# Performance work log

Measured on AMD Instinct MI355X. Metric: run time of the kernel, lower is better.

## Reference

```python
import jax, jax.numpy as jnp
import numpy as np

K = 3  # adaptive kernel size
M = 4  # channel reduction


def setup_inputs() -> dict:
    key = jax.random.key(0)
    ks = jax.random.split(key, 10)
    N, C, H, W = 32, 512, 48, 48
    Cm = C // M            # 128
    P = 512                # planes
    sc = 0.05
    x   = jax.random.normal(ks[0], (N, C, H, W), jnp.float32)
    Wc  = jax.random.normal(ks[1], (Cm, C), jnp.float32) * sc   # conv 1x1 (C->Cm)
    bc  = jax.random.normal(ks[2], (Cm,), jnp.float32) * sc
    Wkk = jax.random.normal(ks[3], (K * K,), jnp.float32) * sc  # conv_kernel (1->k*k, 1x1)
    bkk = jax.random.normal(ks[4], (K * K,), jnp.float32) * sc
    Wck = jax.random.normal(ks[5], (Cm, 2), jnp.float32) * sc   # conv_k (2->Cm, 1x1)
    bck = jax.random.normal(ks[6], (Cm,), jnp.float32) * sc
    b_ad = jax.random.normal(ks[7], (Cm,), jnp.float32) * sc    # conv_adap_kernel bias (learned)
    Wf  = jax.random.normal(ks[8], (P, Cm), jnp.float32) * sc   # fuse 1x1 (Cm->planes)
    bf  = jax.random.normal(ks[9], (P,), jnp.float32) * sc
    return {"x": x, "Wc": Wc, "bc": bc, "Wkk": Wkk, "bkk": bkk,
            "Wck": Wck, "bck": bck, "b_ad": b_ad, "Wf": Wf, "bf": bf}


def reference(x, Wc, bc, Wkk, bkk, Wck, bck, b_ad, Wf, bf):
    N, C, H, W = x.shape
    Cm = Wc.shape[0]
    k = K
    pad = (k - 1) // 2

    # f = relu(conv1x1(x)) -> [N, Cm, H, W]
    f = jax.nn.relu(jnp.einsum('oc,nchw->nohw', Wc, x) + bc[None, :, None, None])

    # global branch: adaptive avg pool to 1 -> shared conv1x1 -> relu -> [N, Cm]
    gk1 = jax.nn.relu(jnp.mean(x, axis=(2, 3)) @ Wc.T + bc)
    # conv_kernel (1->k*k 1x1 over permuted layout): per-channel affine into k*k values
    g_kern = (gk1[:, :, None] * Wkk[None, None, :] + bkk[None, None, :]).reshape(N, Cm, k, k)

    # spatial branch: adaptive max pool to k x k (H,W divisible by k) -> shared conv1x1 -> relu
    xm = x.reshape(N, C, k, H // k, k, W // k).max(axis=(3, 5))  # [N, C, k, k]
    sk = jax.nn.relu(jnp.einsum('oc,nckl->nokl', Wc, xm) + bc[None, :, None, None])

    # kernel generation: conv_k (2->Cm 1x1) over [g_kern, sk], then the permute makes
    # weight[o, c, :, :] = relu(sum_j Wck[o, j] * gs[c, j, :, :] + bck[o])
    gs = jnp.stack([g_kern, sk], axis=2)  # [N, Cm, 2, k, k]
    dynW = jax.nn.relu(jnp.einsum('oj,ncjkl->nockl', Wck, gs)
                       + bck[None, :, None, None, None])  # [N, Cm_out, Cm_in, k, k]

    # per-sample dynamic conv2d, vectorized over batch
    def conv_one(fn, wn):
        return jax.lax.conv_general_dilated(
            fn[None], wn, window_strides=(1, 1),
            padding=[(pad, pad), (pad, pad)])[0]

    y = jax.vmap(conv_one)(f, dynW) + b_ad[None, :, None, None]  # [N, Cm, H, W]

    # fuse 1x1 -> planes
    out = jnp.einsum('oc,nchw->nohw', Wf, y) + bf[None, :, None, None]
    return out
```

## Files before the change

### kernel.cpp

```cpp
#include <hip/hip_runtime.h>

#define N_   32
#define C_   512
#define CM_  128
#define H_   48
#define W_   48
#define HW_  (H_*W_)
#define P_   512

typedef unsigned short ushort_t;
typedef short s8v  __attribute__((ext_vector_type(8)));
typedef float f4v  __attribute__((ext_vector_type(4)));

__device__ __forceinline__ ushort_t f2bf(float x) {
    unsigned int u = __float_as_uint(x);
    u += 0x7fffu + ((u >> 16) & 1u);
    return (ushort_t)(u >> 16);
}

__global__ __launch_bounds__(256) void pool_kernel(const float* __restrict__ x,
                                                   float* __restrict__ meanx,
                                                   float* __restrict__ xm,
                                                   const float* __restrict__ Wc,
                                                   const float* __restrict__ Wf,
                                                   ushort_t* __restrict__ Wc_bf,
                                                   ushort_t* __restrict__ Wf_bf) {
    if (blockIdx.x >= N_ * C_) {
        int idx = (blockIdx.x - N_ * C_) * 256 + threadIdx.x;
        float4 v;
        ushort_t* dst;
        if (idx < 16384) {
            v = ((const float4*)Wc)[idx];
            dst = Wc_bf + (size_t)idx * 4;
        } else {
            int k = idx - 16384;
            v = ((const float4*)Wf)[k];
            dst = Wf_bf + (size_t)k * 4;
        }
        uint2 pk;
        pk.x = (unsigned)f2bf(v.x) | ((unsigned)f2bf(v.y) << 16);
        pk.y = (unsigned)f2bf(v.z) | ((unsigned)f2bf(v.w) << 16);
        *(uint2*)dst = pk;
        return;
    }
    int plane = blockIdx.x;
    const float* base = x + (size_t)plane * HW_;
    int t = threadIdx.x;
    int r = t >> 4, cc = t & 15;
    float sum = 0.f;
    float mx[9];
#pragma unroll
    for (int b = 0; b < 9; ++b) {
        int h = (b / 3) * 16 + r;
        int w = (b % 3) * 16 + cc;
        float v = base[h * W_ + w];
        mx[b] = v;
        sum += v;
    }
#pragma unroll
    for (int off = 32; off > 0; off >>= 1) {
        sum += __shfl_down(sum, off);
#pragma unroll
        for (int b = 0; b < 9; ++b) mx[b] = fmaxf(mx[b], __shfl_down(mx[b], off));
    }
    __shared__ float s[4][10];
    int wave = t >> 6, lane = t & 63;
    if (lane == 0) {
#pragma unroll
        for (int b = 0; b < 9; ++b) s[wave][b] = mx[b];
        s[wave][9] = sum;
    }
    __syncthreads();
    if (t < 9) {
        float v = fmaxf(fmaxf(s[0][t], s[1][t]), fmaxf(s[2][t], s[3][t]));
        xm[(size_t)plane * 9 + t] = v;
    } else if (t == 9) {
        float v = s[0][9] + s[1][9] + s[2][9] + s[3][9];
        meanx[plane] = v * (1.0f / (float)HW_);
    }
}

__global__ __launch_bounds__(512) void branch_kernel(const float* __restrict__ meanx,
                                                     const float* __restrict__ xm,
                                                     const float* __restrict__ Wc,
                                                     const float* __restrict__ bc,
                                                     const float* __restrict__ Wkk,
                                                     const float* __restrict__ bkk,
                                                     float* __restrict__ gs) {
    int n = blockIdx.x;
    __shared__ float sin_[C_ * 10];
    __shared__ float Ws[4][128][17];
    int t = threadIdx.x;
    for (int i = t; i < C_ * 10; i += 512) {
        int c = i / 10, j = i % 10;
        sin_[i] = (j < 9) ? xm[((size_t)n * C_ + c) * 9 + j] : meanx[n * C_ + c];
    }
    int o = t & 127, p = t >> 7;
    float acc[10];
#pragma unroll
    for (int j = 0; j < 10; ++j) acc[j] = 0.f;

    for (int s = 0; s < 8; ++s) {
        __syncthreads();
#pragma unroll
        for (int k = 0; k < 4; ++k) {
            int f = t + k * 512;
            int chunk = f >> 9, oo = (f >> 2) & 127, col4 = f & 3;
            float4 v = *(const float4*)(Wc + (size_t)oo * C_ + chunk * 128 + s * 16 + col4 * 4);
            *(float4*)&Ws[chunk][oo][col4 * 4] = v;
        }
        __syncthreads();
        int cbase = p * 128 + s * 16;
#pragma unroll
        for (int cc = 0; cc < 16; ++cc) {
            float wv = Ws[p][o][cc];
            const float* in = &sin_[(cbase + cc) * 10];
#pragma unroll
            for (int j = 0; j < 10; ++j) acc[j] += wv * in[j];
        }
    }
    __syncthreads();
    float* red = (float*)Ws;
#pragma unroll
    for (int j = 0; j < 10; ++j) red[t * 10 + j] = acc[j];
    __syncthreads();
    if (t < 128) {
        float a[10];
#pragma unroll
        for (int j = 0; j < 10; ++j)
            a[j] = red[t * 10 + j] + red[1280 + t * 10 + j]
                 + red[2560 + t * 10 + j] + red[3840 + t * 10 + j];
        float bco = bc[t];
        float gk1 = fmaxf(a[9] + bco, 0.f);
        size_t gbase = (size_t)n * 18 * CM_;
#pragma unroll
        for (int b = 0; b < 9; ++b) {
            gs[gbase + b * CM_ + t]       = gk1 * Wkk[b] + bkk[b];
            gs[gbase + (9 + b) * CM_ + t] = fmaxf(a[b] + bco, 0.f);
        }
    }
}

__global__ __launch_bounds__(256) void dynw_kernel(const float* __restrict__ gs,
                                                   const float* __restrict__ Wck,
                                                   const float* __restrict__ bck,
                                                   ushort_t* __restrict__ dynW_t) {
    int idx = blockIdx.x * 256 + threadIdx.x;
    int c8 = idx & 15;
    int o  = (idx >> 4) & 127;
    int v  = idx >> 11;
    int r  = v % 9;
    int n  = v / 9;
    const float* gp = gs + ((size_t)n * 18 + r) * CM_ + c8 * 8;
    float w0 = Wck[o * 2], w1 = Wck[o * 2 + 1], bk = bck[o];
    ushort_t u[8];
#pragma unroll
    for (int i = 0; i < 8; ++i) {
        float g = gp[i];
        float s = gp[9 * CM_ + i];
        u[i] = f2bf(fmaxf(w0 * g + w1 * s + bk, 0.f));
    }
    uint4 pk;
    pk.x = (unsigned)u[0] | ((unsigned)u[1] << 16);
    pk.y = (unsigned)u[2] | ((unsigned)u[3] << 16);
    pk.z = (unsigned)u[4] | ((unsigned)u[5] << 16);
    pk.w = (unsigned)u[6] | ((unsigned)u[7] << 16);
    *(uint4*)(dynW_t + (size_t)idx * 8) = pk;
}

__global__ __launch_bounds__(256) void fconv_mfma(const float* __restrict__ x,
                                                  const ushort_t* __restrict__ Wc_bf,
                                                  const float* __restrict__ bc,
                                                  ushort_t* __restrict__ f_t) {
    int n = blockIdx.y;
    int hw0 = blockIdx.x * 64;
    __shared__ ushort_t Bs[64 * 40];
    int t = threadIdx.x;
    int wave = t >> 6, lane = t & 63;
    int j = lane & 15, q = lane >> 4;
    int o_w = wave * 32;
    int sk  = t >> 4;
    int shw = (t & 15) * 4;

    const s8v* A = (const s8v*)Wc_bf;
    f4v acc[2][4];
#pragma unroll
    for (int mt = 0; mt < 2; ++mt)
#pragma unroll
        for (int nt = 0; nt < 4; ++nt) acc[mt][nt] = (f4v){0.f, 0.f, 0.f, 0.f};

    for (int c0 = 0; c0 < C_; c0 += 32) {
        const float* xr = x + ((size_t)n * C_ + c0 + 2 * sk) * HW_ + hw0 + shw;
        float4 v0 = *(const float4*)xr;
        float4 v1 = *(const float4*)(xr + HW_);
        __syncthreads();
        unsigned* Bw = (unsigned*)Bs;
        {
            unsigned w0 = (unsigned)f2bf(v0.x) | ((unsigned)f2bf(v1.x) << 16);
            unsigned w1 = (unsigned)f2bf(v0.y) | ((unsigned)f2bf(v1.y) << 16);
            unsigned w2 = (unsigned)f2bf(v0.z) | ((unsigned)f2bf(v1.z) << 16);
            unsigned w3 = (unsigned)f2bf(v0.w) | ((unsigned)f2bf(v1.w) << 16);
            Bw[(shw + 0) * 20 + sk] = w0;
            Bw[(shw + 1) * 20 + sk] = w1;
            Bw[(shw + 2) * 20 + sk] = w2;
            Bw[(shw + 3) * 20 + sk] = w3;
        }
        __syncthreads();
        s8v a0 = A[(size_t)(o_w + j) * 64 + (c0 >> 3) + q];
        s8v a1 = A[(size_t)(o_w + 16 + j) * 64 + (c0 >> 3) + q];
        s8v b[4];
#pragma unroll
        for (int nt = 0; nt < 4; ++nt)
            b[nt] = *(const s8v*)&Bs[(nt * 16 + j) * 40 + q * 8];
#pragma unroll
        for (int nt = 0; nt < 4; ++nt) {
            acc[0][nt] = __builtin_amdgcn_mfma_f32_16x16x32_bf16(a0, b[nt], acc[0][nt], 0, 0, 0);
            acc[1][nt] = __builtin_amdgcn_mfma_f32_16x16x32_bf16(a1, b[nt], acc[1][nt], 0, 0, 0);
        }
    }
#pragma unroll
    for (int mt = 0; mt < 2; ++mt) {
        int ob = o_w + mt * 16 + q * 4;
        float b4[4];
#pragma unroll
        for (int reg = 0; reg < 4; ++reg) b4[reg] = bc[ob + reg];
#pragma unroll
        for (int nt = 0; nt < 4; ++nt) {
            int hw = hw0 + nt * 16 + j;
            ushort_t u[4];
#pragma unroll
            for (int reg = 0; reg < 4; ++reg)
                u[reg] = f2bf(fmaxf(acc[mt][nt][reg] + b4[reg], 0.f));
            uint2 pk;
            pk.x = (unsigned)u[0] | ((unsigned)u[1] << 16);
            pk.y = (unsigned)u[2] | ((unsigned)u[3] << 16);
            *(uint2*)(f_t + ((size_t)n * HW_ + hw) * CM_ + ob) = pk;
        }
    }
}

__global__ __launch_bounds__(256, 3) void dynconv_mfma(const ushort_t* __restrict__ f_t,
                                                       const ushort_t* __restrict__ dynW_t,
                                                       const float* __restrict__ b_ad,
                                                       ushort_t* __restrict__ y_bf) {
    __shared__ ushort_t Bs[4 * 50 * 128];
    int bid = blockIdx.x;
    int vid = (bid & 7) * 96 + (bid >> 3);
    int n   = vid / 24;
    int h0  = (vid % 24) * 2;
    int t = threadIdx.x;
    int wave = t >> 6, lane = t & 63;
    int j = lane & 15, q = lane >> 4;

    if (t < 128) {
        int ri = t >> 5, wi = ((t >> 4) & 1) * 49, ci = t & 15;
        int off = ((ri * 50 + wi) * 256 + ci * 16) ^ ((wi & 7) << 4);
        uint4 z; z.x = 0u; z.y = 0u; z.z = 0u; z.w = 0u;
        *(uint4*)((char*)Bs + off) = z;
    }
#pragma unroll
    for (int ri = 0; ri < 4; ++ri) {
        int h = h0 - 1 + ri;
        bool hok = (unsigned)h < (unsigned)H_;
        const uint4* src = (const uint4*)(f_t + ((size_t)n * HW_ + h * W_) * CM_);
#pragma unroll
        for (int s = 0; s < 3; ++s) {
            int c2 = s * 256 + t;
            int wi = (c2 >> 4) + 1, ci = c2 & 15;
            uint4 v; v.x = 0u; v.y = 0u; v.z = 0u; v.w = 0u;
            if (hok) v = src[c2];
            int off = ((ri * 50 + wi) * 256 + ci * 16) ^ ((wi & 7) << 4);
            *(uint4*)((char*)Bs + off) = v;
        }
    }
    __syncthreads();

    int ow = wave * 32;
    const s8v* A = (const s8v*)dynW_t;
    size_t abase = ((size_t)n * 9 * 128 + ow + j) * 16 + q;

    f4v acc[2][6];
#pragma unroll
    for (int mt = 0; mt < 2; ++mt)
#pragma unroll
        for (int nt = 0; nt < 6; ++nt) acc[mt][nt] = (f4v){0.f, 0.f, 0.f, 0.f};

    for (int cc = 0; cc < 4; ++cc) {
        s8v a[9][2];
#pragma unroll
        for (int r = 0; r < 9; ++r) {
            a[r][0] = A[abase + (size_t)r * 2048 + cc * 4];
            a[r][1] = A[abase + (size_t)r * 2048 + 256 + cc * 4];
        }
#pragma unroll
        for (int ri = 0; ri < 4; ++ri) {
#pragma unroll
            for (int dwi = 0; dwi < 3; ++dwi) {
                int xr = ((j + dwi) & 7) << 4;
#pragma unroll
                for (int wg = 0; wg < 3; ++wg) {
                    int wi = wg * 16 + j + dwi;
                    int off = ((ri * 50 + wi) * 256 + cc * 64 + q * 16) ^ xr;
                    s8v b = *(const s8v*)((const char*)Bs + off);
                    if (ri < 3) {
                        int r = ri * 3 + dwi;
                        acc[0][wg] = __builtin_amdgcn_mfma_f32_16x16x32_bf16(a[r][0], b, acc[0][wg], 0, 0, 0);
                        acc[1][wg] = __builtin_amdgcn_mfma_f32_16x16x32_bf16(a[r][1], b, acc[1][wg], 0, 0, 0);
                    }
                    if (ri > 0) {
                        int r = (ri - 1) * 3 + dwi;
                        acc[0][3 + wg] = __builtin_amdgcn_mfma_f32_16x16x32_bf16(a[r][0], b, acc[0][3 + wg], 0, 0, 0);
                        acc[1][3 + wg] = __builtin_amdgcn_mfma_f32_16x16x32_bf16(a[r][1], b, acc[1][3 + wg], 0, 0, 0);
                    }
                }
            }
        }
    }

#pragma unroll
    for (int mt = 0; mt < 2; ++mt) {
        int ob = ow + mt * 16 + q * 4;
        float ba[4];
#pragma unroll
        for (int reg = 0; reg < 4; ++reg) ba[reg] = b_ad[ob + reg];
#pragma unroll
        for (int rl = 0; rl < 2; ++rl) {
            int h = h0 + rl;
#pragma unroll
            for (int wg = 0; wg < 3; ++wg) {
                int nt = rl * 3 + wg;
                int hw = h * W_ + wg * 16 + j;
                ushort_t u[4];
#pragma unroll
                for (int reg = 0; reg < 4; ++reg)
                    u[reg] = f2bf(acc[mt][nt][reg] + ba[reg]);
                uint2 pk;
                pk.x = (unsigned)u[0] | ((unsigned)u[1] << 16);
                pk.y = (unsigned)u[2] | ((unsigned)u[3] << 16);
                *(uint2*)(y_bf + ((size_t)n * HW_ + hw) * CM_ + ob) = pk;
            }
        }
    }
}

__global__ __launch_bounds__(128) void fuse_mfma(const ushort_t* __restrict__ y_bf,
                                                 const ushort_t* __restrict__ Wf_bf,
                                                 const float* __restrict__ bf,
                                                 float* __restrict__ out) {
    int n  = blockIdx.z;
    int p0 = blockIdx.y * 64;
    int h0 = blockIdx.x * 4;
    int t = threadIdx.x;
    int wave = t >> 6, lane = t & 63;
    int j = lane & 15, q = lane >> 4;
    int rbase = h0 + wave * 2;

    const s8v* A = (const s8v*)Wf_bf;
    const s8v* B = (const s8v*)y_bf;

    f4v acc[4][6];
#pragma unroll
    for (int mt = 0; mt < 4; ++mt)
#pragma unroll
        for (int nt = 0; nt < 6; ++nt) acc[mt][nt] = (f4v){0.f, 0.f, 0.f, 0.f};

#pragma unroll
    for (int cc = 0; cc < 4; ++cc) {
        s8v a[4];
#pragma unroll
        for (int mt = 0; mt < 4; ++mt)
            a[mt] = A[(size_t)(p0 + mt * 16 + j) * 16 + cc * 4 + q];
        s8v b[6];
#pragma unroll
        for (int rl = 0; rl < 2; ++rl) {
            int h = rbase + rl;
#pragma unroll
            for (int wg = 0; wg < 3; ++wg) {
                int hw = h * W_ + wg * 16 + j;
                b[rl * 3 + wg] = B[((size_t)n * HW_ + hw) * 16 + cc * 4 + q];
            }
        }
#pragma unroll
        for (int mt = 0; mt < 4; ++mt)
#pragma unroll
            for (int nt = 0; nt < 6; ++nt)
                acc[mt][nt] = __builtin_amdgcn_mfma_f32_16x16x32_bf16(
                    a[mt], b[nt], acc[mt][nt], 0, 0, 0);
    }
#pragma unroll
    for (int mt = 0; mt < 4; ++mt) {
        int pb = p0 + mt * 16 + q * 4;
        float b4[4];
#pragma unroll
        for (int reg = 0; reg < 4; ++reg) b4[reg] = bf[pb + reg];
#pragma unroll
        for (int rl = 0; rl < 2; ++rl) {
            int h = rbase + rl;
#pragma unroll
            for (int wg = 0; wg < 3; ++wg) {
                int nt = rl * 3 + wg;
                int hw = h * W_ + wg * 16 + j;
#pragma unroll
                for (int reg = 0; reg < 4; ++reg)
                    out[((size_t)n * P_ + pb + reg) * HW_ + hw] = acc[mt][nt][reg] + b4[reg];
            }
        }
    }
}

extern "C" void kernel_launch(void* const* d_in, const int* in_sizes, int n_in,
                              void* d_out, int out_size, void* d_ws, size_t ws_size,
                              hipStream_t stream) {
    const float* x    = (const float*)d_in[0];
    const float* Wc   = (const float*)d_in[1];
    const float* bc   = (const float*)d_in[2];
    const float* Wkk  = (const float*)d_in[3];
    const float* bkk  = (const float*)d_in[4];
    const float* Wck  = (const float*)d_in[5];
    const float* bck  = (const float*)d_in[6];
    const float* b_ad = (const float*)d_in[7];
    const float* Wf   = (const float*)d_in[8];
    const float* bf   = (const float*)d_in[9];
    float* out = (float*)d_out;

    char* ws = (char*)d_ws;
    float*    meanx  = (float*)(ws);
    float*    xm     = (float*)(ws + 65536);
    float*    gs     = (float*)(ws + 655360);
    ushort_t* dynW_t = (ushort_t*)(ws + 950272);
    ushort_t* f_t    = (ushort_t*)(ws + 10387456);
    ushort_t* y_bf   = (ushort_t*)(ws + 29261824);
    ushort_t* Wc_bf  = (ushort_t*)(ws + 48136192);
    ushort_t* Wf_bf  = (ushort_t*)(ws + 48267264);

    hipLaunchKernelGGL(pool_kernel,    dim3(N_ * C_ + 192), dim3(256), 0, stream,
                       x, meanx, xm, Wc, Wf, Wc_bf, Wf_bf);
    hipLaunchKernelGGL(branch_kernel,  dim3(N_),      dim3(512), 0, stream, meanx, xm, Wc, bc, Wkk, bkk, gs);
    hipLaunchKernelGGL(dynw_kernel,    dim3(2304),    dim3(256), 0, stream, gs, Wck, bck, dynW_t);
    hipLaunchKernelGGL(fconv_mfma,     dim3(36, 32),  dim3(256), 0, stream, x, Wc_bf, bc, f_t);
    hipLaunchKernelGGL(dynconv_mfma,   dim3(768),     dim3(256), 0, stream, f_t, dynW_t, b_ad, y_bf);
    hipLaunchKernelGGL(fuse_mfma,      dim3(12, 8, 32), dim3(128), 0, stream, y_bf, Wf_bf, bf, out);
}
```

Before: 390.7 us.

## Stage y tile in swizzled LDS and widen fuse block over 256 planes

```diff
diff --git a/kernel.cpp b/kernel.cpp
--- a/kernel.cpp
+++ b/kernel.cpp
@@ -343,43 +343,55 @@
     }
 }
 
-__global__ __launch_bounds__(128) void fuse_mfma(const ushort_t* __restrict__ y_bf,
-                                                 const ushort_t* __restrict__ Wf_bf,
-                                                 const float* __restrict__ bf,
-                                                 float* __restrict__ out) {
-    int n  = blockIdx.z;
-    int p0 = blockIdx.y * 64;
-    int h0 = blockIdx.x * 4;
+__global__ __launch_bounds__(256, 3) void fuse_mfma(const ushort_t* __restrict__ y_bf,
+                                                    const ushort_t* __restrict__ Wf_bf,
+                                                    const float* __restrict__ bf,
+                                                    float* __restrict__ out) {
+    __shared__ ushort_t ys[2 * 48 * 128];
+    int bid = blockIdx.x;
+    int vid = (bid & 7) * 192 + (bid >> 3);
+    int n   = vid / 48;
+    int rem = vid % 48;
+    int h0  = (rem >> 1) * 2;
+    int P0  = (rem & 1) * 256;
     int t = threadIdx.x;
     int wave = t >> 6, lane = t & 63;
     int j = lane & 15, q = lane >> 4;
-    int rbase = h0 + wave * 2;
+    int p0w = P0 + wave * 64;
+
+    const uint4* src = (const uint4*)(y_bf + ((size_t)n * HW_ + h0 * W_) * CM_);
+#pragma unroll
+    for (int s = 0; s < 6; ++s) {
+        int c2 = s * 256 + t;
+        int wp = c2 >> 4, ci = c2 & 15;
+        int off = (wp * 256 + ci * 16) ^ ((wp & 7) << 4);
+        *(uint4*)((char*)ys + off) = src[c2];
+    }
+    __syncthreads();
 
     const s8v* A = (const s8v*)Wf_bf;
-    const s8v* B = (const s8v*)y_bf;
-
     f4v acc[4][6];
 #pragma unroll
     for (int mt = 0; mt < 4; ++mt)
 #pragma unroll
         for (int nt = 0; nt < 6; ++nt) acc[mt][nt] = (f4v){0.f, 0.f, 0.f, 0.f};
 
+    int xr = (j & 7) << 4;
 #pragma unroll
     for (int cc = 0; cc < 4; ++cc) {
         s8v a[4];
 #pragma unroll
         for (int mt = 0; mt < 4; ++mt)
-            a[mt] = A[(size_t)(p0 + mt * 16 + j) * 16 + cc * 4 + q];
+            a[mt] = A[(size_t)(p0w + mt * 16 + j) * 16 + cc * 4 + q];
         s8v b[6];
 #pragma unroll
-        for (int rl = 0; rl < 2; ++rl) {
-            int h = rbase + rl;
+        for (int rl = 0; rl < 2; ++rl)
 #pragma unroll
             for (int wg = 0; wg < 3; ++wg) {
-                int hw = h * W_ + wg * 16 + j;
-                b[rl * 3 + wg] = B[((size_t)n * HW_ + hw) * 16 + cc * 4 + q];
+                int wp = rl * 48 + wg * 16 + j;
+                int off = (wp * 256 + cc * 64 + q * 16) ^ xr;
+                b[rl * 3 + wg] = *(const s8v*)((const char*)ys + off);
             }
-        }
 #pragma unroll
         for (int mt = 0; mt < 4; ++mt)
 #pragma unroll
@@ -389,13 +401,13 @@
     }
 #pragma unroll
     for (int mt = 0; mt < 4; ++mt) {
-        int pb = p0 + mt * 16 + q * 4;
+        int pb = p0w + mt * 16 + q * 4;
         float b4[4];
 #pragma unroll
         for (int reg = 0; reg < 4; ++reg) b4[reg] = bf[pb + reg];
 #pragma unroll
         for (int rl = 0; rl < 2; ++rl) {
-            int h = rbase + rl;
+            int h = h0 + rl;
 #pragma unroll
             for (int wg = 0; wg < 3; ++wg) {
                 int nt = rl * 3 + wg;
@@ -439,5 +451,5 @@
     hipLaunchKernelGGL(dynw_kernel,    dim3(2304),    dim3(256), 0, stream, gs, Wck, bck, dynW_t);
     hipLaunchKernelGGL(fconv_mfma,     dim3(36, 32),  dim3(256), 0, stream, x, Wc_bf, bc, f_t);
     hipLaunchKernelGGL(dynconv_mfma,   dim3(768),     dim3(256), 0, stream, f_t, dynW_t, b_ad, y_bf);
-    hipLaunchKernelGGL(fuse_mfma,      dim3(12, 8, 32), dim3(128), 0, stream, y_bf, Wf_bf, bf, out);
-}
+    hipLaunchKernelGGL(fuse_mfma,      dim3(1536),    dim3(256), 0, stream, y_bf, Wf_bf, bf, out);
+}
```

Result: slower. 412.4 us (+5.6%).

## Fuse mean/max pooling into fconv via atomics, removing separate pass over x

Applied to the files above, without the earlier changes.

```diff
diff --git a/kernel.cpp b/kernel.cpp
--- a/kernel.cpp
+++ b/kernel.cpp
@@ -18,15 +18,24 @@
     return (ushort_t)(u >> 16);
 }
 
-__global__ __launch_bounds__(256) void pool_kernel(const float* __restrict__ x,
-                                                   float* __restrict__ meanx,
-                                                   float* __restrict__ xm,
-                                                   const float* __restrict__ Wc,
+__device__ __forceinline__ unsigned fenc(float f) {
+    unsigned u = __float_as_uint(f);
+    return (u & 0x80000000u) ? ~u : (u | 0x80000000u);
+}
+__device__ __forceinline__ float fdec(unsigned k) {
+    unsigned u = (k & 0x80000000u) ? (k ^ 0x80000000u) : ~k;
+    return __uint_as_float(u);
+}
+
+__global__ __launch_bounds__(256) void prep_kernel(const float* __restrict__ Wc,
                                                    const float* __restrict__ Wf,
                                                    ushort_t* __restrict__ Wc_bf,
-                                                   ushort_t* __restrict__ Wf_bf) {
-    if (blockIdx.x >= N_ * C_) {
-        int idx = (blockIdx.x - N_ * C_) * 256 + threadIdx.x;
+                                                   ushort_t* __restrict__ Wf_bf,
+                                                   unsigned* __restrict__ xm_key,
+                                                   float* __restrict__ meanx) {
+    int b = blockIdx.x, t = threadIdx.x;
+    if (b < 128) {
+        int idx = b * 256 + t;
         float4 v;
         ushort_t* dst;
         if (idx < 16384) {
@@ -41,47 +50,15 @@
         pk.x = (unsigned)f2bf(v.x) | ((unsigned)f2bf(v.y) << 16);
         pk.y = (unsigned)f2bf(v.z) | ((unsigned)f2bf(v.w) << 16);
         *(uint2*)dst = pk;
-        return;
-    }
-    int plane = blockIdx.x;
-    const float* base = x + (size_t)plane * HW_;
-    int t = threadIdx.x;
-    int r = t >> 4, cc = t & 15;
-    float sum = 0.f;
-    float mx[9];
-#pragma unroll
-    for (int b = 0; b < 9; ++b) {
-        int h = (b / 3) * 16 + r;
-        int w = (b % 3) * 16 + cc;
-        float v = base[h * W_ + w];
-        mx[b] = v;
-        sum += v;
-    }
-#pragma unroll
-    for (int off = 32; off > 0; off >>= 1) {
-        sum += __shfl_down(sum, off);
-#pragma unroll
-        for (int b = 0; b < 9; ++b) mx[b] = fmaxf(mx[b], __shfl_down(mx[b], off));
-    }
-    __shared__ float s[4][10];
-    int wave = t >> 6, lane = t & 63;
-    if (lane == 0) {
-#pragma unroll
-        for (int b = 0; b < 9; ++b) s[wave][b] = mx[b];
-        s[wave][9] = sum;
-    }
-    __syncthreads();
-    if (t < 9) {
-        float v = fmaxf(fmaxf(s[0][t], s[1][t]), fmaxf(s[2][t], s[3][t]));
-        xm[(size_t)plane * 9 + t] = v;
-    } else if (t == 9) {
-        float v = s[0][9] + s[1][9] + s[2][9] + s[3][9];
-        meanx[plane] = v * (1.0f / (float)HW_);
+    } else if (b < 704) {
+        xm_key[(b - 128) * 256 + t] = 0u;
+    } else {
+        meanx[(b - 704) * 256 + t] = 0.f;
     }
 }
 
 __global__ __launch_bounds__(512) void branch_kernel(const float* __restrict__ meanx,
-                                                     const float* __restrict__ xm,
+                                                     const unsigned* __restrict__ xm_key,
                                                      const float* __restrict__ Wc,
                                                      const float* __restrict__ bc,
                                                      const float* __restrict__ Wkk,
@@ -93,7 +70,8 @@
     int t = threadIdx.x;
     for (int i = t; i < C_ * 10; i += 512) {
         int c = i / 10, j = i % 10;
-        sin_[i] = (j < 9) ? xm[((size_t)n * C_ + c) * 9 + j] : meanx[n * C_ + c];
+        sin_[i] = (j < 9) ? fdec(xm_key[((size_t)n * C_ + c) * 9 + j])
+                          : meanx[n * C_ + c] * (1.0f / (float)HW_);
     }
     int o = t & 127, p = t >> 7;
     float acc[10];
@@ -171,7 +149,9 @@
 __global__ __launch_bounds__(256) void fconv_mfma(const float* __restrict__ x,
                                                   const ushort_t* __restrict__ Wc_bf,
                                                   const float* __restrict__ bc,
-                                                  ushort_t* __restrict__ f_t) {
+                                                  ushort_t* __restrict__ f_t,
+                                                  float* __restrict__ meanx,
+                                                  unsigned* __restrict__ xm_key) {
     int n = blockIdx.y;
     int hw0 = blockIdx.x * 64;
     __shared__ ushort_t Bs[64 * 40];
@@ -182,6 +162,10 @@
     int sk  = t >> 4;
     int shw = (t & 15) * 4;
 
+    int hwa = hw0 + shw;
+    int ha = hwa / 48, wa = hwa % 48;
+    int reg = (ha >> 4) * 3 + (wa >> 4);
+
     const s8v* A = (const s8v*)Wc_bf;
     f4v acc[2][4];
 #pragma unroll
@@ -193,6 +177,32 @@
         const float* xr = x + ((size_t)n * C_ + c0 + 2 * sk) * HW_ + hw0 + shw;
         float4 v0 = *(const float4*)xr;
         float4 v1 = *(const float4*)(xr + HW_);
+
+        float s0 = (v0.x + v0.y) + (v0.z + v0.w);
+        float s1 = (v1.x + v1.y) + (v1.z + v1.w);
+        float m0 = fmaxf(fmaxf(v0.x, v0.y), fmaxf(v0.z, v0.w));
+        float m1 = fmaxf(fmaxf(v1.x, v1.y), fmaxf(v1.z, v1.w));
+#pragma unroll
+        for (int m = 8; m >= 1; m >>= 1) {
+            s0 += __shfl_xor(s0, m);
+            s1 += __shfl_xor(s1, m);
+        }
+#pragma unroll
+        for (int m = 2; m >= 1; m >>= 1) {
+            m0 = fmaxf(m0, __shfl_xor(m0, m));
+            m1 = fmaxf(m1, __shfl_xor(m1, m));
+        }
+        int l16 = t & 15;
+        int c = c0 + 2 * sk;
+        if (l16 == 0) {
+            atomicAdd(&meanx[n * C_ + c], s0);
+            atomicAdd(&meanx[n * C_ + c + 1], s1);
+        }
+        if ((l16 & 3) == 0) {
+            atomicMax(&xm_key[((size_t)(n * C_ + c)) * 9 + reg], fenc(m0));
+            atomicMax(&xm_key[((size_t)(n * C_ + c + 1)) * 9 + reg], fenc(m1));
+        }
+
         __syncthreads();
         unsigned* Bw = (unsigned*)Bs;
         {
@@ -223,14 +233,14 @@
         int ob = o_w + mt * 16 + q * 4;
         float b4[4];
 #pragma unroll
-        for (int reg = 0; reg < 4; ++reg) b4[reg] = bc[ob + reg];
+        for (int r2 = 0; r2 < 4; ++r2) b4[r2] = bc[ob + r2];
 #pragma unroll
         for (int nt = 0; nt < 4; ++nt) {
             int hw = hw0 + nt * 16 + j;
             ushort_t u[4];
 #pragma unroll
-            for (int reg = 0; reg < 4; ++reg)
-                u[reg] = f2bf(fmaxf(acc[mt][nt][reg] + b4[reg], 0.f));
+            for (int r2 = 0; r2 < 4; ++r2)
+                u[r2] = f2bf(fmaxf(acc[mt][nt][r2] + b4[r2], 0.f));
             uint2 pk;
             pk.x = (unsigned)u[0] | ((unsigned)u[1] << 16);
             pk.y = (unsigned)u[2] | ((unsigned)u[3] << 16);
@@ -425,7 +435,7 @@
 
     char* ws = (char*)d_ws;
     float*    meanx  = (float*)(ws);
-    float*    xm     = (float*)(ws + 65536);
+    unsigned* xm_key = (unsigned*)(ws + 65536);
     float*    gs     = (float*)(ws + 655360);
     ushort_t* dynW_t = (ushort_t*)(ws + 950272);
     ushort_t* f_t    = (ushort_t*)(ws + 10387456);
@@ -433,11 +443,13 @@
     ushort_t* Wc_bf  = (ushort_t*)(ws + 48136192);
     ushort_t* Wf_bf  = (ushort_t*)(ws + 48267264);
 
-    hipLaunchKernelGGL(pool_kernel,    dim3(N_ * C_ + 192), dim3(256), 0, stream,
-                       x, meanx, xm, Wc, Wf, Wc_bf, Wf_bf);
-    hipLaunchKernelGGL(branch_kernel,  dim3(N_),      dim3(512), 0, stream, meanx, xm, Wc, bc, Wkk, bkk, gs);
-    hipLaunchKernelGGL(dynw_kernel,    dim3(2304),    dim3(256), 0, stream, gs, Wck, bck, dynW_t);
-    hipLaunchKernelGGL(fconv_mfma,     dim3(36, 32),  dim3(256), 0, stream, x, Wc_bf, bc, f_t);
-    hipLaunchKernelGGL(dynconv_mfma,   dim3(768),     dim3(256), 0, stream, f_t, dynW_t, b_ad, y_bf);
-    hipLaunchKernelGGL(fuse_mfma,      dim3(12, 8, 32), dim3(128), 0, stream, y_bf, Wf_bf, bf, out);
-}
+    hipLaunchKernelGGL(prep_kernel,   dim3(768),     dim3(256), 0, stream,
+                       Wc, Wf, Wc_bf, Wf_bf, xm_key, meanx);
+    hipLaunchKernelGGL(fconv_mfma,    dim3(36, 32),  dim3(256), 0, stream,
+                       x, Wc_bf, bc, f_t, meanx, xm_key);
+    hipLaunchKernelGGL(branch_kernel, dim3(N_),      dim3(512), 0, stream,
+                       meanx, xm_key, Wc, bc, Wkk, bkk, gs);
+    hipLaunchKernelGGL(dynw_kernel,   dim3(2304),    dim3(256), 0, stream, gs, Wck, bck, dynW_t);
+    hipLaunchKernelGGL(dynconv_mfma,  dim3(768),     dim3(256), 0, stream, f_t, dynW_t, b_ad, y_bf);
+    hipLaunchKernelGGL(fuse_mfma,     dim3(12, 8, 32), dim3(128), 0, stream, y_bf, Wf_bf, bf, out);
+}
```

Result: slower. 410.5 us (+5.1%).
